# Kernel optimization log

Hardware: AMD Instinct MI355X
Metric: run time of the kernel (lower is better)

The kernel has to match this reference:

```python
import jax, jax.numpy as jnp
import numpy as np

N_NODES = 50000
N_EDGES = 800000
IN_DIM = 64
HEADS = 8
DHEAD = 8
CLAMP = 5.0


def _xavier(key, shape, fan_in, fan_out):
    std = jnp.sqrt(2.0 / (fan_in + fan_out))
    return std * jax.random.normal(key, shape, dtype=jnp.float32)


def setup_inputs() -> dict:
    key = jax.random.key(0)
    ks = jax.random.split(key, 12)
    HD = HEADS * DHEAD
    x = jax.random.normal(ks[0], (N_NODES, IN_DIM), dtype=jnp.float32)
    edge_attr = jax.random.normal(ks[1], (N_EDGES, IN_DIM), dtype=jnp.float32)
    edge_index = jax.random.randint(ks[2], (2, N_EDGES), 0, N_NODES, dtype=jnp.int32)
    # Linear weights stored as [in, out] so y = x @ W + b
    WQ = _xavier(ks[3], (IN_DIM, HD), IN_DIM, HD)
    bQ = jnp.zeros((HD,), jnp.float32)
    WK = _xavier(ks[4], (IN_DIM, HD), IN_DIM, HD)
    bK = jnp.zeros((HD,), jnp.float32)
    WE = _xavier(ks[5], (IN_DIM, 2 * HD), IN_DIM, 2 * HD)
    bE = jnp.zeros((2 * HD,), jnp.float32)
    WV = _xavier(ks[6], (IN_DIM, HD), IN_DIM, HD)
    bV = jnp.zeros((HD,), jnp.float32)
    Aw = _xavier(ks[7], (DHEAD, HEADS, 1), DHEAD * HEADS, 1)
    VeRow = _xavier(ks[8], (DHEAD, HEADS, DHEAD), DHEAD * HEADS, DHEAD)
    return {"x": x, "edge_attr": edge_attr, "edge_index": edge_index,
            "WQ": WQ, "bQ": bQ, "WK": WK, "bK": bK, "WE": WE, "bE": bE,
            "WV": WV, "bV": bV, "Aw": Aw, "VeRow": VeRow}


def _forward(x, edge_attr, edge_index, WQ, bQ, WK, bK, WE, bE, WV, bV, Aw, VeRow):
    N = x.shape[0]
    src_idx = edge_index[0]
    dst_idx = edge_index[1]
    Q_h = (x @ WQ + bQ).reshape(N, HEADS, DHEAD)
    K_h = (x @ WK + bK).reshape(N, HEADS, DHEAD)
    V_h = (x @ WV + bV).reshape(N, HEADS, DHEAD)
    E = (edge_attr @ WE + bE).reshape(-1, HEADS, 2 * DHEAD)  # [E,H,2D]
    E_w, E_b = E[:, :, :DHEAD], E[:, :, DHEAD:]
    # per-edge score: gather + signed-sqrt transform
    score = K_h[src_idx] + Q_h[dst_idx]              # [E,H,D]
    score = score * E_w
    score = jnp.sqrt(jax.nn.relu(score)) - jnp.sqrt(jax.nn.relu(-score))
    score = score + E_b                               # act = Identity
    e_t = score
    wE = score.reshape(score.shape[0], HEADS * DHEAD)
    # attention logits: contract over head dim with Aw -> [E,H,1]
    logit = jnp.einsum('ehd,dhc->ehc', score, Aw)
    logit = jnp.clip(logit, -CLAMP, CLAMP)
    # segment softmax over destination nodes (pyg_softmax)
    smax = jax.ops.segment_max(logit, dst_idx, num_segments=N)
    ex = jnp.exp(logit - smax[dst_idx])
    denom = jax.ops.segment_sum(ex, dst_idx, num_segments=N)[dst_idx] + 1e-16
    attn = ex / denom                                 # [E,H,1], dropout p=0
    # message passing: scatter-add weighted values
    msg = V_h[src_idx] * attn                         # [E,H,D]
    wV = jax.ops.segment_sum(msg, dst_idx, num_segments=N)
    # edge enhancement
    rowV = jax.ops.segment_sum(e_t * attn, dst_idx, num_segments=N)  # [N,H,D]
    wV = wV + jnp.einsum('nhd,dhc->nhc', rowV, VeRow)
    return wV, wE


def reference(x, edge_attr, edge_index, WQ, bQ, WK, bK, WE, bE, WV, bV, Aw, VeRow):
    return _forward(x, edge_attr, edge_index, WQ, bQ, WK, bK, WE, bE, WV, bV, Aw, VeRow)
```

## Files before the change

kernel.cpp:

```cpp
#include <hip/hip_runtime.h>
#include <hip/hip_bf16.h>
#include <math.h>

#define N_NODES 50000
#define N_EDGES 800000
#define CLAMP_V 5.0f

typedef short short8 __attribute__((ext_vector_type(8)));
typedef float f32x4  __attribute__((ext_vector_type(4)));

static __device__ inline short f2bf(float x) {
    __hip_bfloat16 h = __float2bfloat16(x);
    return __builtin_bit_cast(short, h);
}
static __device__ inline float bf2f(short s) {
    unsigned u = ((unsigned)(unsigned short)s) << 16;
    return __builtin_bit_cast(float, u);
}

__global__ __launch_bounds__(256) void qkv_kernel(
    const float* __restrict__ x,
    const float* __restrict__ WQ, const float* __restrict__ bQ,
    const float* __restrict__ WK, const float* __restrict__ bK,
    const float* __restrict__ WV, const float* __restrict__ bV,
    float* __restrict__ Q, float* __restrict__ K, float* __restrict__ V)
{
    const int t = threadIdx.x;
    const int c = t & 63;
    const int nl = t >> 6;
    const int base = blockIdx.x * 16;

    float accQ[4], accK[4], accV[4];
    int nodes[4];
#pragma unroll
    for (int j = 0; j < 4; ++j) {
        nodes[j] = base + j * 4 + nl;
        accQ[j] = bQ[c]; accK[j] = bK[c]; accV[j] = bV[c];
    }
    for (int k = 0; k < 64; ++k) {
        const float wq = WQ[k * 64 + c];
        const float wk = WK[k * 64 + c];
        const float wv = WV[k * 64 + c];
#pragma unroll
        for (int j = 0; j < 4; ++j) {
            const float xv = x[nodes[j] * 64 + k];
            accQ[j] += xv * wq;
            accK[j] += xv * wk;
            accV[j] += xv * wv;
        }
    }
#pragma unroll
    for (int j = 0; j < 4; ++j) {
        const int n = nodes[j];
        Q[n * 64 + c] = accQ[j];
        K[n * 64 + c] = accK[j];
        V[n * 64 + c] = accV[j];
    }
}

__global__ __launch_bounds__(256, 3) void edge_kernel(
    const float* __restrict__ edge_attr,
    const int* __restrict__ src_idx, const int* __restrict__ dst_idx,
    const float* __restrict__ WE, const float* __restrict__ bE,
    const float* __restrict__ Aw,
    const float* __restrict__ Qn, const float* __restrict__ Kn,
    float* __restrict__ wE_out, float* __restrict__ denom)
{
    __shared__ __align__(16) char raw[40960];
    __shared__ float bEs[128];
    __shared__ float Aws[64];

    short8* Bhi = (short8*)raw;
    short8* Blo = (short8*)(raw + 16384);

    const int t = threadIdx.x;
    const int wave = t >> 6;
    const int lane = t & 63;

    short* BhiE = (short*)raw;
    short* BloE = (short*)(raw + 16384);
    for (int i = t; i < 8192; i += 256) {
        const int j  = i & 7;
        const int ln = (i >> 3) & 63;
        const int kh = (i >> 9) & 1;
        const int ct = i >> 10;
        const int k   = kh * 32 + ((ln >> 4) << 3) + j;
        const int col = (ct << 4) + (ln & 15);
        const float w = WE[k * 128 + col];
        const short hb = f2bf(w);
        BhiE[i] = hb;
        BloE[i] = f2bf(w - bf2f(hb));
    }
    if (t < 128) bEs[t] = bE[t];
    if (t < 64)  Aws[t] = Aw[t];
    __syncthreads();

    float* Ebuf_w = (float*)(raw + 32768 + wave * 2048);

    const int h    = lane >> 3;
    const int kk   = lane & 7;
    const int g    = lane >> 4;
    const int c4   = lane & 15;
    const int h16k = (h << 4) + kk;

    for (int it = blockIdx.x; it < 12500; it += gridDim.x) {
        const int ebase = __builtin_amdgcn_readfirstlane(it * 64 + wave * 16);

        int se[16], de[16];
#pragma unroll
        for (int r = 0; r < 16; ++r) {
            se[r] = src_idx[ebase + r];
            de[r] = dst_idx[ebase + r];
        }

        float4 au[2], av[2];
#pragma unroll
        for (int p = 0; p < 2; ++p) {
            const float* srcp = edge_attr + (size_t)(ebase + c4) * 64 + p * 32 + (g << 3);
            au[p] = *(const float4*)srcp;
            av[p] = *(const float4*)(srcp + 4);
        }

        float kv[16], qv[16];
#pragma unroll
        for (int r = 0; r < 16; ++r) {
            kv[r] = Kn[se[r] * 64 + lane];
            qv[r] = Qn[de[r] * 64 + lane];
        }

        short8 ah[2], al[2];
#pragma unroll
        for (int p = 0; p < 2; ++p) {
            const float xv[8] = {au[p].x, au[p].y, au[p].z, au[p].w,
                                 av[p].x, av[p].y, av[p].z, av[p].w};
#pragma unroll
            for (int j = 0; j < 8; ++j) {
                const short hb = f2bf(xv[j]);
                ah[p][j] = hb;
                al[p][j] = f2bf(xv[j] - bf2f(hb));
            }
        }

        f32x4 acc[8] = {};
#pragma unroll
        for (int kh = 0; kh < 2; ++kh) {
#pragma unroll
            for (int ct = 0; ct < 8; ++ct) {
                const short8 bh = Bhi[(ct * 2 + kh) * 64 + lane];
                const short8 bl = Blo[(ct * 2 + kh) * 64 + lane];
                acc[ct] = __builtin_amdgcn_mfma_f32_16x16x32_bf16(ah[kh], bh, acc[ct], 0, 0, 0);
                acc[ct] = __builtin_amdgcn_mfma_f32_16x16x32_bf16(al[kh], bh, acc[ct], 0, 0, 0);
                acc[ct] = __builtin_amdgcn_mfma_f32_16x16x32_bf16(ah[kh], bl, acc[ct], 0, 0, 0);
            }
        }

#pragma unroll
        for (int q = 0; q < 4; ++q) {
            if (g == q) {
#pragma unroll
                for (int ct = 0; ct < 8; ++ct) {
                    const int col = (ct << 4) + c4;
                    const float b = bEs[col];
                    f32x4 vq = acc[ct];
                    vq[0] += b; vq[1] += b; vq[2] += b; vq[3] += b;
                    *(f32x4*)(Ebuf_w + col * 4) = vq;
                }
            }
            __asm__ volatile("s_waitcnt lgkmcnt(0)" ::: "memory");
            __builtin_amdgcn_sched_barrier(0);
#pragma unroll
            for (int rr = 0; rr < 4; ++rr) {
                const int e = ebase + q * 4 + rr;
                const float kq = kv[q * 4 + rr] + qv[q * 4 + rr];
                const float ew = Ebuf_w[h16k * 4 + rr];
                const float eb = Ebuf_w[(h16k + 8) * 4 + rr];
                float sc = kq * ew;
                sc = copysignf(sqrtf(fabsf(sc)), sc) + eb;
                wE_out[(size_t)e * 64 + lane] = sc;

                float pp = sc * Aws[kk * 8 + h];
                pp += __shfl_xor(pp, 1);
                pp += __shfl_xor(pp, 2);
                pp += __shfl_xor(pp, 4);
                pp = fminf(fmaxf(pp, -CLAMP_V), CLAMP_V);
                const float ex = __expf(pp);
                if (kk == 0) unsafeAtomicAdd(&denom[de[q * 4 + rr] * 8 + h], ex);
            }
            __builtin_amdgcn_sched_barrier(0);
        }
    }
}

__global__ __launch_bounds__(256) void scatter_kernel(
    const int* __restrict__ src_idx, const int* __restrict__ dst_idx,
    const float* __restrict__ Vn, const float* __restrict__ wE_out,
    const float* __restrict__ denom,
    const float* __restrict__ Aw, const float* __restrict__ VeRow,
    float* __restrict__ wV_out)
{
    __shared__ float VeL[512];
    __shared__ float AwL[64];
    const int t = threadIdx.x;
    if (t < 64) AwL[t] = Aw[t];
    for (int i = t; i < 512; i += 256) VeL[i] = VeRow[i];
    __syncthreads();

    const int wave = t >> 6;
    const int lane = t & 63;
    const int h = lane >> 3;
    const int kk = lane & 7;
    const int totalWaves = gridDim.x * 4;

    for (int e = blockIdx.x * 4 + wave; e < N_EDGES; e += totalWaves) {
        const int s = src_idx[e];
        const int d = dst_idx[e];
        const float et = wE_out[(size_t)e * 64 + lane];

        float p = et * AwL[kk * 8 + h];
        p += __shfl_xor(p, 1);
        p += __shfl_xor(p, 2);
        p += __shfl_xor(p, 4);
        p = fminf(fmaxf(p, -CLAMP_V), CLAMP_V);
        const float ex = __expf(p);
        const float dn = denom[(size_t)d * 8 + h];
        const float attn = ex / (dn + 1e-16f);

        const float vv = Vn[(size_t)s * 64 + lane];
        float rsum = 0.f;
#pragma unroll
        for (int dd = 0; dd < 8; ++dd) {
            const float etd = __shfl(et, (lane & 56) + dd);
            rsum += etd * VeL[dd * 64 + lane];
        }
        unsafeAtomicAdd(&wV_out[(size_t)d * 64 + lane], attn * (vv + rsum));
    }
}

extern "C" void kernel_launch(void* const* d_in, const int* in_sizes, int n_in,
                              void* d_out, int out_size, void* d_ws, size_t ws_size,
                              hipStream_t stream) {
    const float* x         = (const float*)d_in[0];
    const float* edge_attr = (const float*)d_in[1];
    const int*   ei        = (const int*)  d_in[2];
    const float* WQ = (const float*)d_in[3];
    const float* bQ = (const float*)d_in[4];
    const float* WK = (const float*)d_in[5];
    const float* bK = (const float*)d_in[6];
    const float* WE = (const float*)d_in[7];
    const float* bE = (const float*)d_in[8];
    const float* WV = (const float*)d_in[9];
    const float* bV = (const float*)d_in[10];
    const float* Aw = (const float*)d_in[11];
    const float* VeRow = (const float*)d_in[12];

    float* out    = (float*)d_out;
    float* wV_out = out;
    float* wE_out = out + (size_t)N_NODES * 64;

    float* ws    = (float*)d_ws;
    float* Q     = ws;
    float* K     = ws + 3200000;
    float* V     = ws + 6400000;
    float* denom = ws + 9600000;

    const int* src_idx = ei;
    const int* dst_idx = ei + N_EDGES;

    hipMemsetAsync(wV_out, 0, (size_t)N_NODES * 64 * sizeof(float), stream);
    hipMemsetAsync(denom, 0, (size_t)N_NODES * 8 * sizeof(float), stream);

    qkv_kernel<<<3125, 256, 0, stream>>>(x, WQ, bQ, WK, bK, WV, bV, Q, K, V);
    edge_kernel<<<768, 256, 0, stream>>>(edge_attr, src_idx, dst_idx, WE, bE, Aw,
                                         Q, K, wE_out, denom);
    scatter_kernel<<<2048, 256, 0, stream>>>(src_idx, dst_idx, V, wE_out, denom,
                                             Aw, VeRow, wV_out);
}
```

Measured before the change: 394.4 us.

## Fuse scatter into edge kernel by accumulating unnormalized messages, normalize afterward

The message scatter now happens inside the edge kernel: it gathers V per edge, computes the VeRow edge-enhancement term, and atomically adds exp(logit)-weighted messages into the output. A small finalize kernel then divides by the per-node denominator. This removes the second pass that re-read wE, src/dst and recomputed logits, at the cost of more registers and atomics in the edge kernel. It also relies on the softmax being shift-free, which holds because logits are clamped.

```diff
diff --git a/kernel.cpp b/kernel.cpp
--- a/kernel.cpp
+++ b/kernel.cpp
@@ -64,11 +64,14 @@
     const float* __restrict__ WE, const float* __restrict__ bE,
     const float* __restrict__ Aw,
     const float* __restrict__ Qn, const float* __restrict__ Kn,
-    float* __restrict__ wE_out, float* __restrict__ denom)
+    const float* __restrict__ Vn, const float* __restrict__ VeRow,
+    float* __restrict__ wE_out, float* __restrict__ denom,
+    float* __restrict__ wV_num)
 {
     __shared__ __align__(16) char raw[40960];
     __shared__ float bEs[128];
     __shared__ float Aws[64];
+    __shared__ float VeL[512];
 
     short8* Bhi = (short8*)raw;
     short8* Blo = (short8*)(raw + 16384);
@@ -93,6 +96,7 @@
     }
     if (t < 128) bEs[t] = bE[t];
     if (t < 64)  Aws[t] = Aw[t];
+    for (int i = t; i < 512; i += 256) VeL[i] = VeRow[i];
     __syncthreads();
 
     float* Ebuf_w = (float*)(raw + 32768 + wave * 2048);
@@ -121,11 +125,12 @@
             av[p] = *(const float4*)(srcp + 4);
         }
 
-        float kv[16], qv[16];
+        float kv[16], qv[16], vv[16];
 #pragma unroll
         for (int r = 0; r < 16; ++r) {
             kv[r] = Kn[se[r] * 64 + lane];
             qv[r] = Qn[de[r] * 64 + lane];
+            vv[r] = Vn[se[r] * 64 + lane];
         }
 
         short8 ah[2], al[2];
@@ -171,6 +176,7 @@
 #pragma unroll
             for (int rr = 0; rr < 4; ++rr) {
                 const int e = ebase + q * 4 + rr;
+                const int d = de[q * 4 + rr];
                 const float kq = kv[q * 4 + rr] + qv[q * 4 + rr];
                 const float ew = Ebuf_w[h16k * 4 + rr];
                 const float eb = Ebuf_w[(h16k + 8) * 4 + rr];
@@ -184,56 +190,30 @@
                 pp += __shfl_xor(pp, 4);
                 pp = fminf(fmaxf(pp, -CLAMP_V), CLAMP_V);
                 const float ex = __expf(pp);
-                if (kk == 0) unsafeAtomicAdd(&denom[de[q * 4 + rr] * 8 + h], ex);
+                if (kk == 0) unsafeAtomicAdd(&denom[d * 8 + h], ex);
+
+                float rsum = 0.f;
+#pragma unroll
+                for (int dd = 0; dd < 8; ++dd) {
+                    const float etd = __shfl(sc, (lane & 56) + dd);
+                    rsum += etd * VeL[dd * 64 + lane];
+                }
+                unsafeAtomicAdd(&wV_num[(size_t)d * 64 + lane],
+                                ex * (vv[q * 4 + rr] + rsum));
             }
             __builtin_amdgcn_sched_barrier(0);
         }
     }
 }
 
-__global__ __launch_bounds__(256) void scatter_kernel(
-    const int* __restrict__ src_idx, const int* __restrict__ dst_idx,
-    const float* __restrict__ Vn, const float* __restrict__ wE_out,
-    const float* __restrict__ denom,
-    const float* __restrict__ Aw, const float* __restrict__ VeRow,
-    float* __restrict__ wV_out)
+__global__ __launch_bounds__(256) void finalize_kernel(
+    const float* __restrict__ denom, float* __restrict__ wV)
 {
-    __shared__ float VeL[512];
-    __shared__ float AwL[64];
-    const int t = threadIdx.x;
-    if (t < 64) AwL[t] = Aw[t];
-    for (int i = t; i < 512; i += 256) VeL[i] = VeRow[i];
-    __syncthreads();
-
-    const int wave = t >> 6;
-    const int lane = t & 63;
-    const int h = lane >> 3;
-    const int kk = lane & 7;
-    const int totalWaves = gridDim.x * 4;
-
-    for (int e = blockIdx.x * 4 + wave; e < N_EDGES; e += totalWaves) {
-        const int s = src_idx[e];
-        const int d = dst_idx[e];
-        const float et = wE_out[(size_t)e * 64 + lane];
-
-        float p = et * AwL[kk * 8 + h];
-        p += __shfl_xor(p, 1);
-        p += __shfl_xor(p, 2);
-        p += __shfl_xor(p, 4);
-        p = fminf(fmaxf(p, -CLAMP_V), CLAMP_V);
-        const float ex = __expf(p);
-        const float dn = denom[(size_t)d * 8 + h];
-        const float attn = ex / (dn + 1e-16f);
-
-        const float vv = Vn[(size_t)s * 64 + lane];
-        float rsum = 0.f;
-#pragma unroll
-        for (int dd = 0; dd < 8; ++dd) {
-            const float etd = __shfl(et, (lane & 56) + dd);
-            rsum += etd * VeL[dd * 64 + lane];
-        }
-        unsafeAtomicAdd(&wV_out[(size_t)d * 64 + lane], attn * (vv + rsum));
-    }
+    const int i = blockIdx.x * 256 + threadIdx.x;
+    const int n = i >> 6;
+    const int h = (i >> 3) & 7;
+    const float dn = denom[n * 8 + h] + 1e-16f;
+    wV[i] = wV[i] / dn;
 }
 
 extern "C" void kernel_launch(void* const* d_in, const int* in_sizes, int n_in,
@@ -271,7 +251,6 @@
 
     qkv_kernel<<<3125, 256, 0, stream>>>(x, WQ, bQ, WK, bK, WV, bV, Q, K, V);
     edge_kernel<<<768, 256, 0, stream>>>(edge_attr, src_idx, dst_idx, WE, bE, Aw,
-                                         Q, K, wE_out, denom);
-    scatter_kernel<<<2048, 256, 0, stream>>>(src_idx, dst_idx, V, wE_out, denom,
-                                             Aw, VeRow, wV_out);
-}
+                                         Q, K, V, VeRow, wE_out, denom, wV_out);
+    finalize_kernel<<<12500, 256, 0, stream>>>(denom, wV_out);
+}
```

Result: faster. 335.7 us (-14.9%).
